# Performance work log

Measured on AMD Instinct MI355X. Metric: run time of the kernel, lower is better.

Reference implementation:

```python
import jax, jax.numpy as jnp
import numpy as np

INPUT_WINDOW = 2048
HEAD_DIM = 128  # embedding_size // number_of_heads = 2048 // 16
TAU = 1.0
SCALE = 1.0 / ((INPUT_WINDOW * HEAD_DIM) ** 0.5 * TAU)


def setup_inputs() -> dict:
    key = jax.random.key(0)
    # (batch, number_of_series, length_input_window, hidden_dimensionality)
    x = jax.random.normal(key, (8, 16, 2048, 128), dtype=jnp.float32)
    return {"x": x}


def reference(x) -> jnp.ndarray:
    # Q = K = V = x; scores: [B, S, W, W]
    qk = jnp.einsum("bswd,bsud->bswu", x, x) * SCALE
    attn = jax.nn.softmax(qk, axis=-1)
    # dropout(p=0.1) is identity in eval mode
    out = jnp.einsum("bswu,bsud->bswd", attn, x)
    return out
```

## Files before the change

kernel.cpp:

```cpp
#include <hip/hip_runtime.h>
#include <hip/hip_bf16.h>


#define NSEQ   2048
#define DIM    128
#define KVBLK  64
#define TILES  (NSEQ / KVBLK)
#define IMG    (KVBLK * DIM)
#define EC (1.44269504088896f / 512.0f)

typedef short s8v __attribute__((ext_vector_type(8)));
typedef float f4   __attribute__((ext_vector_type(4)));
typedef float f16v __attribute__((ext_vector_type(16)));
typedef unsigned int u2 __attribute__((ext_vector_type(2)));
typedef unsigned int u4 __attribute__((ext_vector_type(4)));

typedef __attribute__((address_space(1))) const void glob_t;
typedef __attribute__((address_space(3))) void lds_t;

__device__ __forceinline__ unsigned pk2(float a, float b) {
    union { __hip_bfloat162 h; unsigned u; } c;
    c.h = __float22bfloat162_rn(make_float2(a, b));
    return c.u;
}
__device__ __forceinline__ int swz(int r) { return ((r & 7) ^ ((r >> 3) & 7)) << 3; }

__global__ __launch_bounds__(256)
void prepass(const float* __restrict__ x, short* __restrict__ wsK,
             short* __restrict__ wsV) {
    const int b = blockIdx.x;
    const float* src = x + (size_t)b * IMG;
    short* dK = wsK + (size_t)b * IMG;
    short* dV = wsV + (size_t)b * IMG;
    const int rw = threadIdx.x >> 4;
    const int cg = threadIdx.x & 15;

    f4 ld[8];
    const float* s = src + (size_t)(4 * rw) * DIM + 8 * cg;
#pragma unroll
    for (int i = 0; i < 4; ++i) {
        ld[2*i]   = *(const f4*)(s + i * DIM);
        ld[2*i+1] = *(const f4*)(s + i * DIM + 4);
    }
#pragma unroll
    for (int i = 0; i < 4; ++i) {
        const int r = 4 * rw + i;
        u4 kv = { pk2(ld[2*i][0],   ld[2*i][1]),   pk2(ld[2*i][2],   ld[2*i][3]),
                  pk2(ld[2*i+1][0], ld[2*i+1][1]), pk2(ld[2*i+1][2], ld[2*i+1][3]) };
        *(u4*)&dK[(r * DIM + 8 * cg) ^ swz(r)] = kv;
    }
#pragma unroll
    for (int j = 0; j < 8; ++j) {
        const int d  = 8 * cg + j;
        const int hi = j >> 2, jj = j & 3;
        u2 vv = { pk2(ld[0 + hi][jj], ld[2 + hi][jj]),
                  pk2(ld[4 + hi][jj], ld[6 + hi][jj]) };
        *(u2*)&dV[(d * KVBLK + 4 * rw) ^ swz(d)] = vv;
    }
}

__global__ __launch_bounds__(256, 2)
void attn_lds(const float* __restrict__ x, const short* __restrict__ wsK,
              const short* __restrict__ wsV, float* __restrict__ out) {
    const int bid  = blockIdx.x;
    const int wg   = (bid & 7) * 256 + (bid >> 3);
    const int head = wg >> 4;
    const int qb   = wg & 15;

    const float* __restrict__ xh = x   + (size_t)head * (NSEQ * DIM);
    float* __restrict__       oh = out + (size_t)head * (NSEQ * DIM);
    const short* gK = wsK + (size_t)head * TILES * IMG;
    const short* gV = wsV + (size_t)head * TILES * IMG;

    const int tid  = threadIdx.x;
    const int lane = tid & 63;
    const int wave = tid >> 6;
    const int l31  = lane & 31;
    const int h    = lane >> 5;

    __shared__ __align__(16) short sK [2][IMG];
    __shared__ __align__(16) short sVt[2][IMG];

    const int qw0 = qb * 128 + wave * 32;
    s8v Qf[8];
    {
        const float* qp = xh + (size_t)(qw0 + l31) * DIM + 8 * h;
#pragma unroll
        for (int ks = 0; ks < 8; ++ks) {
            f4 a = *(const f4*)(qp + ks * 16);
            f4 b = *(const f4*)(qp + ks * 16 + 4);
            u4 q = { pk2(a[0] * EC, a[1] * EC), pk2(a[2] * EC, a[3] * EC),
                     pk2(b[0] * EC, b[1] * EC), pk2(b[2] * EC, b[3] * EC) };
            Qf[ks] = *(s8v*)&q;
        }
    }

    f16v accO[4];
#pragma unroll
    for (int dt = 0; dt < 4; ++dt) accO[dt] = (f16v)(0.f);
    float lsum = 0.f;

    const int so = wave * 512 + lane * 8;
    auto stage = [&](int b, int t) {
        const short* srcK = gK + (size_t)t * IMG + so;
        const short* srcV = gV + (size_t)t * IMG + so;
#pragma unroll
        for (int i = 0; i < 4; ++i) {
            __builtin_amdgcn_global_load_lds((glob_t*)(srcK + i * 2048),
                (lds_t*)&sK[b][wave * 512 + i * 2048], 16, 0, 0);
            __builtin_amdgcn_global_load_lds((glob_t*)(srcV + i * 2048),
                (lds_t*)&sVt[b][wave * 512 + i * 2048], 16, 0, 0);
        }
    };

    stage(0, 0);
    __syncthreads();
    int buf = 0;

    for (int t = 0; t < TILES; ++t) {
        if (t + 1 < TILES) stage(buf ^ 1, t + 1);

        f16v accS[2];
        accS[0] = (f16v)(0.f); accS[1] = (f16v)(0.f);
        __builtin_amdgcn_s_setprio(1);
#pragma unroll
        for (int ut = 0; ut < 2; ++ut) {
            const int r    = ut * 32 + l31;
            const int base = (r * DIM + 8 * h);
            const int sz   = swz(r);
#pragma unroll
            for (int ks = 0; ks < 8; ++ks) {
                s8v Kf = *(const s8v*)&sK[buf][(base + ks * 16) ^ sz];
                accS[ut] = __builtin_amdgcn_mfma_f32_32x32x16_bf16(
                    Kf, Qf[ks], accS[ut], 0, 0, 0);
            }
        }
        __builtin_amdgcn_s_setprio(0);

        float part = 0.f;
#pragma unroll
        for (int ut = 0; ut < 2; ++ut)
#pragma unroll
            for (int r = 0; r < 16; ++r) {
                float v = __builtin_amdgcn_exp2f(accS[ut][r]);
                accS[ut][r] = v;
                part += v;
            }
        lsum += part;

        s8v Pf[4];
#pragma unroll
        for (int ks = 0; ks < 4; ++ks) {
#define PP(f) accS[(f) >> 4][(f) & 15]
            unsigned pa0 = pk2(PP(8*ks + 0), PP(8*ks + 1));
            unsigned pa1 = pk2(PP(8*ks + 2), PP(8*ks + 3));
            unsigned pb0 = pk2(PP(8*ks + 4), PP(8*ks + 5));
            unsigned pb1 = pk2(PP(8*ks + 6), PP(8*ks + 7));
#undef PP
            auto t0 = __builtin_amdgcn_permlane32_swap(pa0, pb0, false, false);
            auto t1 = __builtin_amdgcn_permlane32_swap(pa1, pb1, false, false);
            u4 w = { (unsigned)t0[0], (unsigned)t1[0], (unsigned)t0[1], (unsigned)t1[1] };
            Pf[ks] = *(s8v*)&w;
        }

        __builtin_amdgcn_s_setprio(1);
#pragma unroll
        for (int dt = 0; dt < 4; ++dt) {
            const int d    = dt * 32 + l31;
            const int base = d * KVBLK + 8 * h;
            const int sz   = swz(d);
#pragma unroll
            for (int ks = 0; ks < 4; ++ks) {
                s8v Vf = *(const s8v*)&sVt[buf][(base + ks * 16) ^ sz];
                accO[dt] = __builtin_amdgcn_mfma_f32_32x32x16_bf16(
                    Pf[ks], Vf, accO[dt], 0, 0, 0);
            }
        }
        __builtin_amdgcn_s_setprio(0);

        __syncthreads();
        buf ^= 1;
    }

    const float tot = lsum + __shfl_xor(lsum, 32);
    const float inv = 1.f / tot;
#pragma unroll
    for (int r = 0; r < 16; ++r) {
        const int q      = (r & 3) + 8 * (r >> 2) + 4 * h;
        const float invq = __shfl(inv, q, 32);
        float* op = oh + (size_t)(qw0 + q) * DIM + l31;
#pragma unroll
        for (int dt = 0; dt < 4; ++dt)
            op[dt * 32] = accO[dt][r] * invq;
    }
}

__global__ __launch_bounds__(256, 2)
void attn_fwd_fb(const float* __restrict__ x, float* __restrict__ out) {
    const int bid  = blockIdx.x;
    const int wg   = (bid & 7) * 256 + (bid >> 3);
    const int head = wg >> 4;
    const int qb   = wg & 15;
    const float* __restrict__ xh = x   + (size_t)head * (NSEQ * DIM);
    float* __restrict__       oh = out + (size_t)head * (NSEQ * DIM);
    const int tid  = threadIdx.x;
    const int lane = tid & 63;
    const int wave = tid >> 6;
    const int l31  = lane & 31;
    const int h    = lane >> 5;
    __shared__ __align__(16) short sK [KVBLK * DIM];
    __shared__ __align__(16) short sVt[DIM * KVBLK];
    const int qw0 = qb * 128 + wave * 32;
    s8v Qf[8];
    {
        const float* qp = xh + (size_t)(qw0 + l31) * DIM + 8 * h;
#pragma unroll
        for (int ks = 0; ks < 8; ++ks) {
            f4 a = *(const f4*)(qp + ks * 16);
            f4 b = *(const f4*)(qp + ks * 16 + 4);
            u4 q = { pk2(a[0] * EC, a[1] * EC), pk2(a[2] * EC, a[3] * EC),
                     pk2(b[0] * EC, b[1] * EC), pk2(b[2] * EC, b[3] * EC) };
            Qf[ks] = *(s8v*)&q;
        }
    }
    f16v accO[4];
#pragma unroll
    for (int dt = 0; dt < 4; ++dt) accO[dt] = (f16v)(0.f);
    float lsum = 0.f;
    const int rw = tid >> 4;
    const int cg = tid & 15;
    f4 ld[8];
    {
        const float* s = xh + (size_t)(4 * rw) * DIM + 8 * cg;
#pragma unroll
        for (int i = 0; i < 4; ++i) {
            ld[2*i]   = *(const f4*)(s + i * DIM);
            ld[2*i+1] = *(const f4*)(s + i * DIM + 4);
        }
    }
    for (int kv0 = 0; kv0 < NSEQ; kv0 += KVBLK) {
#pragma unroll
        for (int i = 0; i < 4; ++i) {
            const int r = 4 * rw + i;
            u4 kv = { pk2(ld[2*i][0],   ld[2*i][1]),   pk2(ld[2*i][2],   ld[2*i][3]),
                      pk2(ld[2*i+1][0], ld[2*i+1][1]), pk2(ld[2*i+1][2], ld[2*i+1][3]) };
            *(u4*)&sK[(r * DIM + 8 * cg) ^ swz(r)] = kv;
        }
#pragma unroll
        for (int j = 0; j < 8; ++j) {
            const int d  = 8 * cg + j;
            const int hi = j >> 2, jj = j & 3;
            u2 vv = { pk2(ld[0 + hi][jj], ld[2 + hi][jj]),
                      pk2(ld[4 + hi][jj], ld[6 + hi][jj]) };
            *(u2*)&sVt[(d * KVBLK + 4 * rw) ^ swz(d)] = vv;
        }
        __syncthreads();
        f16v accS[2];
        accS[0] = (f16v)(0.f); accS[1] = (f16v)(0.f);
        __builtin_amdgcn_s_setprio(1);
#pragma unroll
        for (int ut = 0; ut < 2; ++ut) {
            const int r    = ut * 32 + l31;
            const int base = r * DIM + 8 * h;
            const int sz   = swz(r);
#pragma unroll
            for (int ks = 0; ks < 8; ++ks) {
                s8v Kf = *(const s8v*)&sK[(base + ks * 16) ^ sz];
                accS[ut] = __builtin_amdgcn_mfma_f32_32x32x16_bf16(
                    Kf, Qf[ks], accS[ut], 0, 0, 0);
            }
        }
        __builtin_amdgcn_s_setprio(0);
        if (kv0 + KVBLK < NSEQ) {
            const float* s = xh + (size_t)(kv0 + KVBLK + 4 * rw) * DIM + 8 * cg;
#pragma unroll
            for (int i = 0; i < 4; ++i) {
                ld[2*i]   = *(const f4*)(s + i * DIM);
                ld[2*i+1] = *(const f4*)(s + i * DIM + 4);
            }
        }
        float part = 0.f;
#pragma unroll
        for (int ut = 0; ut < 2; ++ut)
#pragma unroll
            for (int r = 0; r < 16; ++r) {
                float v = __builtin_amdgcn_exp2f(accS[ut][r]);
                accS[ut][r] = v;
                part += v;
            }
        lsum += part;
        s8v Pf[4];
#pragma unroll
        for (int ks = 0; ks < 4; ++ks) {
#define PP(f) accS[(f) >> 4][(f) & 15]
            unsigned pa0 = pk2(PP(8*ks + 0), PP(8*ks + 1));
            unsigned pa1 = pk2(PP(8*ks + 2), PP(8*ks + 3));
            unsigned pb0 = pk2(PP(8*ks + 4), PP(8*ks + 5));
            unsigned pb1 = pk2(PP(8*ks + 6), PP(8*ks + 7));
#undef PP
            auto t0 = __builtin_amdgcn_permlane32_swap(pa0, pb0, false, false);
            auto t1 = __builtin_amdgcn_permlane32_swap(pa1, pb1, false, false);
            u4 w = { (unsigned)t0[0], (unsigned)t1[0], (unsigned)t0[1], (unsigned)t1[1] };
            Pf[ks] = *(s8v*)&w;
        }
        __builtin_amdgcn_s_setprio(1);
#pragma unroll
        for (int dt = 0; dt < 4; ++dt) {
            const int d    = dt * 32 + l31;
            const int base = d * KVBLK + 8 * h;
            const int sz   = swz(d);
#pragma unroll
            for (int ks = 0; ks < 4; ++ks) {
                s8v Vf = *(const s8v*)&sVt[(base + ks * 16) ^ sz];
                accO[dt] = __builtin_amdgcn_mfma_f32_32x32x16_bf16(
                    Pf[ks], Vf, accO[dt], 0, 0, 0);
            }
        }
        __builtin_amdgcn_s_setprio(0);
        __syncthreads();
    }
    const float tot = lsum + __shfl_xor(lsum, 32);
    const float inv = 1.f / tot;
#pragma unroll
    for (int r = 0; r < 16; ++r) {
        const int q      = (r & 3) + 8 * (r >> 2) + 4 * h;
        const float invq = __shfl(inv, q, 32);
        float* op = oh + (size_t)(qw0 + q) * DIM + l31;
#pragma unroll
        for (int dt = 0; dt < 4; ++dt)
            op[dt * 32] = accO[dt][r] * invq;
    }
}

extern "C" void kernel_launch(void* const* d_in, const int* in_sizes, int n_in,
                              void* d_out, int out_size, void* d_ws, size_t ws_size,
                              hipStream_t stream) {
    const float* x = (const float*)d_in[0];
    float* out     = (float*)d_out;
    const size_t need = (size_t)2 * 128 * TILES * IMG * sizeof(short);
    if (ws_size >= need) {
        short* wsK = (short*)d_ws;
        short* wsV = wsK + (size_t)128 * TILES * IMG;
        hipLaunchKernelGGL(prepass, dim3(128 * TILES), dim3(256), 0, stream, x, wsK, wsV);
        hipLaunchKernelGGL(attn_lds, dim3(2048), dim3(256), 0, stream, x, wsK, wsV, out);
    } else {
        hipLaunchKernelGGL(attn_fwd_fb, dim3(2048), dim3(256), 0, stream, x, out);
    }
}
```

Measured before the change: 362.5 us.

## Process 64 query rows per wave to reuse K/V fragments across two tiles

Each wave now handles two 32-row query tiles instead of one, so every K and V fragment read from LDS feeds two MFMAs, and the grid is halved to 1024 blocks. This halves LDS read traffic and K/V staging per query row. The S tile is processed in two 32-column halves to limit live registers. The cost is more accumulator registers (two sets of O accumulators plus S), which risks spills or lower occupancy under the 2-blocks-per-SM bound, and a smaller grid with less parallelism.

```diff
diff --git a/kernel.cpp b/kernel.cpp
--- a/kernel.cpp
+++ b/kernel.cpp
@@ -60,12 +60,12 @@
 }
 
 __global__ __launch_bounds__(256, 2)
-void attn_lds(const float* __restrict__ x, const short* __restrict__ wsK,
-              const short* __restrict__ wsV, float* __restrict__ out) {
+void attn_lds64(const float* __restrict__ x, const short* __restrict__ wsK,
+                const short* __restrict__ wsV, float* __restrict__ out) {
     const int bid  = blockIdx.x;
-    const int wg   = (bid & 7) * 256 + (bid >> 3);
-    const int head = wg >> 4;
-    const int qb   = wg & 15;
+    const int wg   = (bid & 7) * 128 + (bid >> 3);
+    const int head = wg >> 3;
+    const int qb   = wg & 7;
 
     const float* __restrict__ xh = x   + (size_t)head * (NSEQ * DIM);
     float* __restrict__       oh = out + (size_t)head * (NSEQ * DIM);
@@ -81,24 +81,27 @@
     __shared__ __align__(16) short sK [2][IMG];
     __shared__ __align__(16) short sVt[2][IMG];
 
-    const int qw0 = qb * 128 + wave * 32;
-    s8v Qf[8];
-    {
-        const float* qp = xh + (size_t)(qw0 + l31) * DIM + 8 * h;
+    const int qw0 = qb * 256 + wave * 64;
+    s8v Qf[2][8];
+#pragma unroll
+    for (int qt = 0; qt < 2; ++qt) {
+        const float* qp = xh + (size_t)(qw0 + qt * 32 + l31) * DIM + 8 * h;
 #pragma unroll
         for (int ks = 0; ks < 8; ++ks) {
             f4 a = *(const f4*)(qp + ks * 16);
             f4 b = *(const f4*)(qp + ks * 16 + 4);
             u4 q = { pk2(a[0] * EC, a[1] * EC), pk2(a[2] * EC, a[3] * EC),
                      pk2(b[0] * EC, b[1] * EC), pk2(b[2] * EC, b[3] * EC) };
-            Qf[ks] = *(s8v*)&q;
-        }
-    }
-
-    f16v accO[4];
-#pragma unroll
-    for (int dt = 0; dt < 4; ++dt) accO[dt] = (f16v)(0.f);
-    float lsum = 0.f;
+            Qf[qt][ks] = *(s8v*)&q;
+        }
+    }
+
+    f16v accO[2][4];
+#pragma unroll
+    for (int qt = 0; qt < 2; ++qt)
+#pragma unroll
+        for (int dt = 0; dt < 4; ++dt) accO[qt][dt] = (f16v)(0.f);
+    float lsum[2] = {0.f, 0.f};
 
     const int so = wave * 512 + lane * 8;
     auto stage = [&](int b, int t) {
@@ -120,78 +123,88 @@
     for (int t = 0; t < TILES; ++t) {
         if (t + 1 < TILES) stage(buf ^ 1, t + 1);
 
-        f16v accS[2];
-        accS[0] = (f16v)(0.f); accS[1] = (f16v)(0.f);
-        __builtin_amdgcn_s_setprio(1);
 #pragma unroll
         for (int ut = 0; ut < 2; ++ut) {
-            const int r    = ut * 32 + l31;
-            const int base = (r * DIM + 8 * h);
-            const int sz   = swz(r);
-#pragma unroll
-            for (int ks = 0; ks < 8; ++ks) {
-                s8v Kf = *(const s8v*)&sK[buf][(base + ks * 16) ^ sz];
-                accS[ut] = __builtin_amdgcn_mfma_f32_32x32x16_bf16(
-                    Kf, Qf[ks], accS[ut], 0, 0, 0);
-            }
-        }
-        __builtin_amdgcn_s_setprio(0);
-
-        float part = 0.f;
-#pragma unroll
-        for (int ut = 0; ut < 2; ++ut)
-#pragma unroll
-            for (int r = 0; r < 16; ++r) {
-                float v = __builtin_amdgcn_exp2f(accS[ut][r]);
-                accS[ut][r] = v;
-                part += v;
-            }
-        lsum += part;
-
-        s8v Pf[4];
-#pragma unroll
-        for (int ks = 0; ks < 4; ++ks) {
-#define PP(f) accS[(f) >> 4][(f) & 15]
-            unsigned pa0 = pk2(PP(8*ks + 0), PP(8*ks + 1));
-            unsigned pa1 = pk2(PP(8*ks + 2), PP(8*ks + 3));
-            unsigned pb0 = pk2(PP(8*ks + 4), PP(8*ks + 5));
-            unsigned pb1 = pk2(PP(8*ks + 6), PP(8*ks + 7));
+            f16v accS[2];
+            accS[0] = (f16v)(0.f); accS[1] = (f16v)(0.f);
+            {
+                const int r    = ut * 32 + l31;
+                const int base = r * DIM + 8 * h;
+                const int sz   = swz(r);
+                __builtin_amdgcn_s_setprio(1);
+#pragma unroll
+                for (int ks = 0; ks < 8; ++ks) {
+                    s8v Kf = *(const s8v*)&sK[buf][(base + ks * 16) ^ sz];
+                    accS[0] = __builtin_amdgcn_mfma_f32_32x32x16_bf16(
+                        Kf, Qf[0][ks], accS[0], 0, 0, 0);
+                    accS[1] = __builtin_amdgcn_mfma_f32_32x32x16_bf16(
+                        Kf, Qf[1][ks], accS[1], 0, 0, 0);
+                }
+                __builtin_amdgcn_s_setprio(0);
+            }
+
+            s8v Pf[2][2];
+#pragma unroll
+            for (int qt = 0; qt < 2; ++qt) {
+                float part = 0.f;
+#pragma unroll
+                for (int r = 0; r < 16; ++r) {
+                    float v = __builtin_amdgcn_exp2f(accS[qt][r]);
+                    accS[qt][r] = v;
+                    part += v;
+                }
+                lsum[qt] += part;
+#pragma unroll
+                for (int ksl = 0; ksl < 2; ++ksl) {
+#define PP(f) accS[qt][(f) & 15]
+                    unsigned pa0 = pk2(PP(8*ksl + 0), PP(8*ksl + 1));
+                    unsigned pa1 = pk2(PP(8*ksl + 2), PP(8*ksl + 3));
+                    unsigned pb0 = pk2(PP(8*ksl + 4), PP(8*ksl + 5));
+                    unsigned pb1 = pk2(PP(8*ksl + 6), PP(8*ksl + 7));
 #undef PP
-            auto t0 = __builtin_amdgcn_permlane32_swap(pa0, pb0, false, false);
-            auto t1 = __builtin_amdgcn_permlane32_swap(pa1, pb1, false, false);
-            u4 w = { (unsigned)t0[0], (unsigned)t1[0], (unsigned)t0[1], (unsigned)t1[1] };
-            Pf[ks] = *(s8v*)&w;
-        }
-
-        __builtin_amdgcn_s_setprio(1);
-#pragma unroll
-        for (int dt = 0; dt < 4; ++dt) {
-            const int d    = dt * 32 + l31;
-            const int base = d * KVBLK + 8 * h;
-            const int sz   = swz(d);
-#pragma unroll
-            for (int ks = 0; ks < 4; ++ks) {
-                s8v Vf = *(const s8v*)&sVt[buf][(base + ks * 16) ^ sz];
-                accO[dt] = __builtin_amdgcn_mfma_f32_32x32x16_bf16(
-                    Pf[ks], Vf, accO[dt], 0, 0, 0);
-            }
-        }
-        __builtin_amdgcn_s_setprio(0);
+                    auto t0 = __builtin_amdgcn_permlane32_swap(pa0, pb0, false, false);
+                    auto t1 = __builtin_amdgcn_permlane32_swap(pa1, pb1, false, false);
+                    u4 w = { (unsigned)t0[0], (unsigned)t1[0],
+                             (unsigned)t0[1], (unsigned)t1[1] };
+                    Pf[qt][ksl] = *(s8v*)&w;
+                }
+            }
+
+            __builtin_amdgcn_s_setprio(1);
+#pragma unroll
+            for (int dt = 0; dt < 4; ++dt) {
+                const int d    = dt * 32 + l31;
+                const int base = d * KVBLK + 8 * h;
+                const int sz   = swz(d);
+#pragma unroll
+                for (int ksl = 0; ksl < 2; ++ksl) {
+                    s8v Vf = *(const s8v*)&sVt[buf][(base + (2 * ut + ksl) * 16) ^ sz];
+                    accO[0][dt] = __builtin_amdgcn_mfma_f32_32x32x16_bf16(
+                        Pf[0][ksl], Vf, accO[0][dt], 0, 0, 0);
+                    accO[1][dt] = __builtin_amdgcn_mfma_f32_32x32x16_bf16(
+                        Pf[1][ksl], Vf, accO[1][dt], 0, 0, 0);
+                }
+            }
+            __builtin_amdgcn_s_setprio(0);
+        }
 
         __syncthreads();
         buf ^= 1;
     }
 
-    const float tot = lsum + __shfl_xor(lsum, 32);
-    const float inv = 1.f / tot;
-#pragma unroll
-    for (int r = 0; r < 16; ++r) {
-        const int q      = (r & 3) + 8 * (r >> 2) + 4 * h;
-        const float invq = __shfl(inv, q, 32);
-        float* op = oh + (size_t)(qw0 + q) * DIM + l31;
-#pragma unroll
-        for (int dt = 0; dt < 4; ++dt)
-            op[dt * 32] = accO[dt][r] * invq;
+#pragma unroll
+    for (int qt = 0; qt < 2; ++qt) {
+        const float tot = lsum[qt] + __shfl_xor(lsum[qt], 32);
+        const float inv = 1.f / tot;
+#pragma unroll
+        for (int r = 0; r < 16; ++r) {
+            const int q      = (r & 3) + 8 * (r >> 2) + 4 * h;
+            const float invq = __shfl(inv, q, 32);
+            float* op = oh + (size_t)(qw0 + qt * 32 + q) * DIM + l31;
+#pragma unroll
+            for (int dt = 0; dt < 4; ++dt)
+                op[dt * 32] = accO[qt][dt][r] * invq;
+        }
     }
 }
 
@@ -342,7 +355,7 @@
         short* wsK = (short*)d_ws;
         short* wsV = wsK + (size_t)128 * TILES * IMG;
         hipLaunchKernelGGL(prepass, dim3(128 * TILES), dim3(256), 0, stream, x, wsK, wsV);
-        hipLaunchKernelGGL(attn_lds, dim3(2048), dim3(256), 0, stream, x, wsK, wsV, out);
+        hipLaunchKernelGGL(attn_lds64, dim3(1024), dim3(256), 0, stream, x, wsK, wsV, out);
     } else {
         hipLaunchKernelGGL(attn_fwd_fb, dim3(2048), dim3(256), 0, stream, x, out);
     }
```

Result: slower. 996.7 us (+174.9%).
